# Performance work log

Measured on AMD Instinct MI355X. Metric: run time of the kernel, lower is better.

Reference implementation:

```python
import jax, jax.numpy as jnp
import numpy as np


def setup_inputs() -> dict:
    key = jax.random.key(0)
    k1, k2, k3 = jax.random.split(key, 3)
    B, C, S, D = 8, 256, 2048, 64
    a = jax.random.normal(k1, (B, C, S), dtype=jnp.float32)
    b = jax.random.normal(k2, (B, S, D), dtype=jnp.float32)
    c = jax.random.normal(k3, (B, S, D), dtype=jnp.float32)
    return {"a": a, "b": b, "c": c}


def reference(a, b, c):
    # mid[b, n, m] = softmax_m(b @ c^T), unscaled
    scores = jnp.einsum("bnd,bmd->bnm", b, c)
    mid = jax.nn.softmax(scores, axis=-1)  # [B, S, S]
    # out = a @ mid^T + a  -> [B, C, S]
    out = jnp.einsum("bcm,bnm->bcn", a, mid) + a
    return out
```

## Files before the change

### kernel.cpp

```cpp
#include <hip/hip_runtime.h>
#include <stdint.h>

#define S 2048
#define DHEAD 64
#define CDIM 256
#define NBATCH 8
#define NSTEP 32
#define SMT 8

typedef __attribute__((ext_vector_type(4))) float f32x4;
typedef __attribute__((ext_vector_type(8))) short s16x8;
typedef __attribute__((ext_vector_type(8))) _Float16 f16x8;
typedef __attribute__((ext_vector_type(4))) unsigned short u16x4;

static __device__ __forceinline__ unsigned short f2bf(float f) {
    unsigned int u = __builtin_bit_cast(unsigned int, f);
    unsigned int r = (u + 0x7FFFu + ((u >> 16) & 1u)) >> 16;
    return (unsigned short)r;
}
static __device__ __forceinline__ unsigned short f2h(float f) {
    _Float16 h = (_Float16)f;
    return __builtin_bit_cast(unsigned short, h);
}
static __device__ __forceinline__ float bf2f(unsigned short u) {
    return __builtin_bit_cast(float, (unsigned int)u << 16);
}

#define GLOAD16(g, l)                                                              \
    __builtin_amdgcn_global_load_lds(                                              \
        (const __attribute__((address_space(1))) void*)(g),                        \
        (__attribute__((address_space(3))) void*)(l), 16, 0, 0)

__global__ __launch_bounds__(256) void cvt_kernel(
    const float* __restrict__ a, const float* __restrict__ b, const float* __restrict__ c,
    unsigned short* __restrict__ a16, unsigned short* __restrict__ b16,
    unsigned short* __restrict__ c16)
{
    const int na4 = NBATCH * CDIM * S / 4;
    const int nbc4 = NBATCH * S * DHEAD / 4;
    int i0 = blockIdx.x * 256 + threadIdx.x;
    int stride = gridDim.x * 256;
    for (int i = i0; i < na4; i += stride) {
        f32x4 v = ((const f32x4*)a)[i];
        u16x4 o; o.x = f2bf(v.x); o.y = f2bf(v.y); o.z = f2bf(v.z); o.w = f2bf(v.w);
        ((u16x4*)a16)[i] = o;
    }
    for (int i = i0; i < nbc4; i += stride) {
        f32x4 v = ((const f32x4*)b)[i];
        u16x4 o; o.x = f2h(v.x); o.y = f2h(v.y); o.z = f2h(v.z); o.w = f2h(v.w);
        ((u16x4*)b16)[i] = o;
        f32x4 u = ((const f32x4*)c)[i];
        u16x4 p; p.x = f2h(u.x); p.y = f2h(u.y); p.z = f2h(u.z); p.w = f2h(u.w);
        ((u16x4*)c16)[i] = p;
    }
}

__global__ __launch_bounds__(256, 2) void scores_kernel(
    const unsigned short* __restrict__ B16, const unsigned short* __restrict__ C16,
    unsigned short* __restrict__ E, float* __restrict__ Lp, int b0, int nb)
{
    const int bid = blockIdx.x;
    int lb, idx;
    if (nb == 8) { lb = bid & 7; idx = bid >> 3; }
    else { lb = bid / 64; idx = bid - lb * 64; }
    const int gb = b0 + lb;
    const int nt = idx >> 1, mh = idx & 1;
    const int n0 = nt * 64;
    const int mbase = mh * (SMT * 128);

    const unsigned short* __restrict__ bp = B16 + (size_t)gb * S * DHEAD;
    const unsigned short* __restrict__ cp = C16 + (size_t)gb * S * DHEAD;
    unsigned short* __restrict__ Ep = E + (size_t)lb * S * S;

    __shared__ unsigned short bs[64 * 64];
    __shared__ unsigned short cs[2][128 * 64];
    __shared__ unsigned short es[64 * 136];
    __shared__ float Lsh[4 * 32];

    const int tid = threadIdx.x;
    const int lane = tid & 63;
    const int w = tid >> 6;
    const int wr = w >> 1, wc = w & 1;
    const int q = lane >> 4, r15 = lane & 15;

    int cRow[4], cOff[4], cR_[4], bRow[2], bOff[2], bR_[2];
    #pragma unroll
    for (int t = 0; t < 4; ++t) {
        int r = w + 4 * t, ch = r * 64 + lane;
        cR_[t] = r; cRow[t] = ch >> 3;
        cOff[t] = ((ch & 7) ^ ((ch >> 3) & 7)) * 8;
    }
    #pragma unroll
    for (int t = 0; t < 2; ++t) {
        int r = w + 4 * t, ch = r * 64 + lane;
        bR_[t] = r; bRow[t] = ch >> 3;
        bOff[t] = ((ch & 7) ^ ((ch >> 3) & 7)) * 8;
    }

#define SSTAGE_C(buf, m0)                                                          \
    {                                                                              \
        _Pragma("unroll")                                                          \
        for (int t = 0; t < 4; ++t)                                                \
            GLOAD16(cp + (size_t)((m0) + cRow[t]) * DHEAD + cOff[t],               \
                    &cs[buf][cR_[t] * 512]);                                       \
    }

    #pragma unroll
    for (int t = 0; t < 2; ++t)
        GLOAD16(bp + (size_t)(n0 + bRow[t]) * DHEAD + bOff[t], &bs[bR_[t] * 512]);
    SSTAGE_C(0, mbase);

    float sj[2] = {0.f, 0.f};

    #pragma unroll
    for (int mt = 0; mt < SMT; ++mt) {
        const int cur = mt & 1;
        const int m0 = mbase + mt * 128;
        if (mt < SMT - 1) {
            SSTAGE_C(cur ^ 1, m0 + 128);
            asm volatile("s_waitcnt vmcnt(4)" ::: "memory");
        } else {
            asm volatile("s_waitcnt vmcnt(0)" ::: "memory");
        }
        __builtin_amdgcn_sched_barrier(0);
        __builtin_amdgcn_s_barrier();
        __builtin_amdgcn_sched_barrier(0);

        f32x4 acc[4][2] = {};
        #pragma unroll
        for (int kk = 0; kk < 2; ++kk) {
            const int sz = ((kk * 4 + q) ^ (r15 & 7)) * 8;
            f16x8 af[4], bf[2];
            #pragma unroll
            for (int i = 0; i < 4; ++i)
                af[i] = *(const f16x8*)&cs[cur][(wr * 64 + i * 16 + r15) * 64 + sz];
            #pragma unroll
            for (int j = 0; j < 2; ++j)
                bf[j] = *(const f16x8*)&bs[(wc * 32 + j * 16 + r15) * 64 + sz];
            __builtin_amdgcn_s_setprio(1);
            #pragma unroll
            for (int i = 0; i < 4; ++i)
                #pragma unroll
                for (int j = 0; j < 2; ++j)
                    acc[i][j] = __builtin_amdgcn_mfma_f32_16x16x32_f16(af[i], bf[j], acc[i][j], 0, 0, 0);
            __builtin_amdgcn_s_setprio(0);
        }

        u16x4 pk[4][2];
        #pragma unroll
        for (int i = 0; i < 4; ++i)
            #pragma unroll
            for (int j = 0; j < 2; ++j) {
                float e0 = __expf(acc[i][j][0]);
                float e1 = __expf(acc[i][j][1]);
                float e2 = __expf(acc[i][j][2]);
                float e3 = __expf(acc[i][j][3]);
                sj[j] += (e0 + e1) + (e2 + e3);
                pk[i][j].x = f2bf(e0); pk[i][j].y = f2bf(e1);
                pk[i][j].z = f2bf(e2); pk[i][j].w = f2bf(e3);
            }

        __syncthreads();
        #pragma unroll
        for (int i = 0; i < 4; ++i)
            #pragma unroll
            for (int j = 0; j < 2; ++j) {
                int nl = wc * 32 + j * 16 + r15;
                int ml = wr * 64 + i * 16 + q * 4;
                *(u16x4*)&es[nl * 136 + ml] = pk[i][j];
            }
        __syncthreads();

        #pragma unroll
        for (int t = 0; t < 4; ++t) {
            int ch = tid + 256 * t;
            int row = ch >> 4, off = ch & 15;
            f32x4 v = *(const f32x4*)&es[row * 136 + off * 8];
            *(f32x4*)&Ep[(size_t)(n0 + row) * S + m0 + off * 8] = v;
        }
    }
#undef SSTAGE_C

    #pragma unroll
    for (int j = 0; j < 2; ++j) {
        sj[j] += __shfl_xor(sj[j], 16);
        sj[j] += __shfl_xor(sj[j], 32);
    }
    if (lane < 16) {
        Lsh[w * 32 + r15] = sj[0];
        Lsh[w * 32 + 16 + r15] = sj[1];
    }
    __syncthreads();
    if (tid < 64) {
        int wcn = tid >> 5, rem = tid & 31;
        float s = Lsh[wcn * 32 + rem] + Lsh[(2 + wcn) * 32 + rem];
        Lp[((size_t)lb * 2 + mh) * S + n0 + tid] = s;
    }
}

#define GEMM_DECODE()                                                             \
    const int tid = threadIdx.x;                                                  \
    const int lane = tid & 63;                                                    \
    const int w = tid >> 6;                                                       \
    const int wr = w >> 1, wc = w & 1;                                            \
    const int q = lane >> 4, r15 = lane & 15;                                     \
    int aRow[4], aOff[4], aR_[4], bRow[2], bOff[2], bR_[2];                       \
    _Pragma("unroll")                                                             \
    for (int t = 0; t < 4; ++t) {                                                 \
        int r = w + 4 * t, ch = r * 64 + lane;                                    \
        aR_[t] = r; aRow[t] = ch >> 3;                                            \
        aOff[t] = ((ch & 7) ^ ((ch >> 3) & 7)) * 8;                               \
    }                                                                             \
    _Pragma("unroll")                                                             \
    for (int t = 0; t < 2; ++t) {                                                 \
        int r = w + 4 * t, ch = r * 64 + lane;                                    \
        bR_[t] = r; bRow[t] = ch >> 3;                                            \
        bOff[t] = ((ch & 7) ^ ((ch >> 3) & 7)) * 8;                               \
    }

#define STAGEP(bufA, bufB, k0)                                                    \
    {                                                                             \
        _Pragma("unroll")                                                         \
        for (int t = 0; t < 4; ++t)                                               \
            GLOAD16(Ap + (size_t)(c0 + aRow[t]) * S + (k0) + aOff[t],             \
                    (bufA) + aR_[t] * 512);                                       \
        _Pragma("unroll")                                                         \
        for (int t = 0; t < 2; ++t)                                               \
            GLOAD16(Bp + (size_t)(n0 + bRow[t]) * S + (k0) + bOff[t],             \
                    (bufB) + bR_[t] * 512);                                       \
    }

#define GEMM_EPILOGUE()                                                           \
    float rcpL[2];                                                                \
    _Pragma("unroll")                                                             \
    for (int j = 0; j < 2; ++j) {                                                 \
        int n = n0 + wc * 32 + j * 16 + r15;                                      \
        float s = Lp[(size_t)lb * 2 * S + n] + Lp[((size_t)lb * 2 + 1) * S + n]; \
        rcpL[j] = 1.0f / s;                                                       \
    }                                                                             \
    _Pragma("unroll")                                                             \
    for (int i = 0; i < 4; ++i) {                                                 \
        _Pragma("unroll")                                                         \
        for (int rr = 0; rr < 4; ++rr) {                                          \
            int cc = c0 + wr * 64 + i * 16 + q * 4 + rr;                          \
            size_t base = (size_t)cc * S;                                         \
            _Pragma("unroll")                                                     \
            for (int j = 0; j < 2; ++j) {                                         \
                int n = n0 + wc * 32 + j * 16 + r15;                              \
                op[base + n] = acc[i][j][rr] * rcpL[j] + bf2f(Ap[base + n]);      \
            }                                                                     \
        }                                                                         \
    }

__global__ __launch_bounds__(256, 2) void gemm_kernel3(
    const unsigned short* __restrict__ a16, const unsigned short* __restrict__ E,
    const float* __restrict__ Lp, float* __restrict__ out, int b0, int nb)
{
    const int bid = blockIdx.x;
    int lb, idx;
    if (nb == 8) { lb = bid & 7; idx = bid >> 3; }
    else { lb = bid / 64; idx = bid - lb * 64; }
    const int gb = b0 + lb;
    const int nt = idx >> 1, ct = idx & 1;
    const int n0 = nt * 64, c0 = ct * 128;

    const unsigned short* __restrict__ Ap = a16 + (size_t)gb * CDIM * S;
    const unsigned short* __restrict__ Bp = E + (size_t)lb * S * S;
    float* __restrict__ op = out + (size_t)gb * CDIM * S;

    extern __shared__ char gsm[];
    unsigned short* As[3];
    unsigned short* Bs[3];
    #pragma unroll
    for (int u = 0; u < 3; ++u) {
        As[u] = (unsigned short*)gsm + u * (128 * 64 + 64 * 64);
        Bs[u] = As[u] + 128 * 64;
    }

    GEMM_DECODE();

    f32x4 acc[4][2] = {};

    STAGEP(As[0], Bs[0], 0);
    STAGEP(As[1], Bs[1], 64);

    const int sw0 = (q ^ (r15 & 7)) * 8;
    const int sw1 = ((4 + q) ^ (r15 & 7)) * 8;

    #pragma unroll
    for (int kt = 0; kt < NSTEP; ++kt) {
        const int cur = kt % 3;
        if (kt <= NSTEP - 3) {
            STAGEP(As[(kt + 2) % 3], Bs[(kt + 2) % 3], (kt + 2) * 64);
            asm volatile("s_waitcnt vmcnt(12)" ::: "memory");
        } else if (kt == NSTEP - 2) {
            asm volatile("s_waitcnt vmcnt(6)" ::: "memory");
        } else {
            asm volatile("s_waitcnt vmcnt(0)" ::: "memory");
        }
        __builtin_amdgcn_sched_barrier(0);
        __builtin_amdgcn_s_barrier();
        __builtin_amdgcn_sched_barrier(0);

        const unsigned short* Ar = As[cur];
        const unsigned short* Br = Bs[cur];
        #pragma unroll
        for (int kk = 0; kk < 2; ++kk) {
            const int sz = kk ? sw1 : sw0;
            s16x8 af[4], bf[2];
            #pragma unroll
            for (int i = 0; i < 4; ++i)
                af[i] = *(const s16x8*)&Ar[(wr * 64 + i * 16 + r15) * 64 + sz];
            #pragma unroll
            for (int j = 0; j < 2; ++j)
                bf[j] = *(const s16x8*)&Br[(wc * 32 + j * 16 + r15) * 64 + sz];
            __builtin_amdgcn_s_setprio(1);
            #pragma unroll
            for (int i = 0; i < 4; ++i)
                #pragma unroll
                for (int j = 0; j < 2; ++j)
                    acc[i][j] = __builtin_amdgcn_mfma_f32_16x16x32_bf16(af[i], bf[j], acc[i][j], 0, 0, 0);
            __builtin_amdgcn_s_setprio(0);
        }

        __builtin_amdgcn_sched_barrier(0);
        __builtin_amdgcn_s_barrier();
    }

    GEMM_EPILOGUE();
}

__global__ __launch_bounds__(256, 2) void gemm_kernel2(
    const unsigned short* __restrict__ a16, const unsigned short* __restrict__ E,
    const float* __restrict__ Lp, float* __restrict__ out, int b0, int nb)
{
    const int bid = blockIdx.x;
    int lb, idx;
    if (nb == 8) { lb = bid & 7; idx = bid >> 3; }
    else { lb = bid / 64; idx = bid - lb * 64; }
    const int gb = b0 + lb;
    const int nt = idx >> 1, ct = idx & 1;
    const int n0 = nt * 64, c0 = ct * 128;

    const unsigned short* __restrict__ Ap = a16 + (size_t)gb * CDIM * S;
    const unsigned short* __restrict__ Bp = E + (size_t)lb * S * S;
    float* __restrict__ op = out + (size_t)gb * CDIM * S;

    __shared__ unsigned short AsS[2][128 * 64];
    __shared__ unsigned short BsS[2][64 * 64];

    GEMM_DECODE();

    f32x4 acc[4][2] = {};

    STAGEP(AsS[0], BsS[0], 0);
    __syncthreads();

    const int sw0 = (q ^ (r15 & 7)) * 8;
    const int sw1 = ((4 + q) ^ (r15 & 7)) * 8;

    #pragma unroll 2
    for (int kt = 0; kt < NSTEP; ++kt) {
        const int cur = kt & 1;
        if (kt < NSTEP - 1) STAGEP(AsS[cur ^ 1], BsS[cur ^ 1], (kt + 1) * 64);

        #pragma unroll
        for (int kk = 0; kk < 2; ++kk) {
            const int sz = kk ? sw1 : sw0;
            s16x8 af[4], bf[2];
            #pragma unroll
            for (int i = 0; i < 4; ++i)
                af[i] = *(const s16x8*)&AsS[cur][(wr * 64 + i * 16 + r15) * 64 + sz];
            #pragma unroll
            for (int j = 0; j < 2; ++j)
                bf[j] = *(const s16x8*)&BsS[cur][(wc * 32 + j * 16 + r15) * 64 + sz];
            #pragma unroll
            for (int i = 0; i < 4; ++i)
                #pragma unroll
                for (int j = 0; j < 2; ++j)
                    acc[i][j] = __builtin_amdgcn_mfma_f32_16x16x32_bf16(af[i], bf[j], acc[i][j], 0, 0, 0);
        }
        __syncthreads();
    }

    GEMM_EPILOGUE();
}

extern "C" void kernel_launch(void* const* d_in, const int* in_sizes, int n_in,
                              void* d_out, int out_size, void* d_ws, size_t ws_size,
                              hipStream_t stream) {
    const float* a = (const float*)d_in[0];
    const float* b = (const float*)d_in[1];
    const float* c = (const float*)d_in[2];
    float* out = (float*)d_out;

    const size_t a16_bytes = (size_t)NBATCH * CDIM * S * 2;
    const size_t bc_bytes = (size_t)NBATCH * S * DHEAD * 2;
    const size_t head = a16_bytes + 2 * bc_bytes;
    const size_t perb = (size_t)S * S * 2 + (size_t)2 * S * 4;
    int G = 1;
    if (ws_size > head + perb) {
        size_t g = (ws_size - head) / perb;
        G = (g >= NBATCH) ? NBATCH : (int)g;
        if (G < 1) G = 1;
    }
    unsigned short* a16 = (unsigned short*)d_ws;
    unsigned short* b16 = (unsigned short*)((char*)d_ws + a16_bytes);
    unsigned short* c16 = (unsigned short*)((char*)d_ws + a16_bytes + bc_bytes);
    unsigned short* E = (unsigned short*)((char*)d_ws + head);
    float* Lp = (float*)((char*)d_ws + head + (size_t)G * S * S * 2);

    const int gemm_lds3 = 3 * (128 * 64 + 64 * 64) * 2;
    hipError_t attr_ok = hipFuncSetAttribute(
        reinterpret_cast<const void*>(gemm_kernel3),
        hipFuncAttributeMaxDynamicSharedMemorySize, gemm_lds3);

    cvt_kernel<<<1024, 256, 0, stream>>>(a, b, c, a16, b16, c16);

    for (int b0 = 0; b0 < NBATCH; b0 += G) {
        int nb = (NBATCH - b0 < G) ? (NBATCH - b0) : G;
        scores_kernel<<<64 * nb, 256, 0, stream>>>(b16, c16, E, Lp, b0, nb);
        if (attr_ok == hipSuccess)
            gemm_kernel3<<<64 * nb, 256, gemm_lds3, stream>>>(a16, E, Lp, out, b0, nb);
        else
            gemm_kernel2<<<64 * nb, 256, 0, stream>>>(a16, E, Lp, out, b0, nb);
    }
}
```

Before: 50.68 us.

## Replace GEMM with full-C wide-tile kernel using split-K waves and register A

Adds a 512-thread GEMM kernel in which each block covers all 256 C rows for a 64-column output tile, so each E tile is read once instead of twice. The A operand is loaded straight from global memory into registers and double-buffered there, while only the E tile is staged through a 3-deep LDS ring. The two wave groups each handle half of every K step, and their partial sums are reduced through LDS before the epilogue. This halves the grid and drops the old no-LDS fallback kernel, trading lower E traffic for larger register pressure, non-coalesced A loads and an added reduction step.

```diff
diff --git a/kernel.cpp b/kernel.cpp
--- a/kernel.cpp
+++ b/kernel.cpp
@@ -195,6 +195,123 @@
         int wcn = tid >> 5, rem = tid & 31;
         float s = Lsh[wcn * 32 + rem] + Lsh[(2 + wcn) * 32 + rem];
         Lp[((size_t)lb * 2 + mh) * S + n0 + tid] = s;
+    }
+}
+
+__global__ __launch_bounds__(512, 2) void gemm_kernelW(
+    const unsigned short* __restrict__ a16, const unsigned short* __restrict__ E,
+    const float* __restrict__ Lp, float* __restrict__ out, int b0, int nb)
+{
+    const int bid = blockIdx.x;
+    int lb, nt;
+    if (nb == 8) { lb = bid & 7; nt = bid >> 3; }
+    else { lb = bid / 32; nt = bid - lb * 32; }
+    const int gb = b0 + lb;
+    const int n0 = nt * 64;
+
+    const unsigned short* __restrict__ Ap = a16 + (size_t)gb * CDIM * S;
+    const unsigned short* __restrict__ Bp = E + (size_t)lb * S * S;
+    float* __restrict__ op = out + (size_t)gb * CDIM * S;
+
+    extern __shared__ char gsm[];
+    unsigned short* const Bbase = (unsigned short*)gsm;
+
+    const int tid = threadIdx.x;
+    const int lane = tid & 63;
+    const int w = tid >> 6;
+    const int wr = w & 3, ks = w >> 2;
+    const int q = lane >> 4, r15 = lane & 15;
+
+    const int brow = tid >> 3;
+    const int bsw = ((tid & 7) ^ (brow & 7)) * 8;
+    const size_t bgl = (size_t)(n0 + brow) * S + bsw;
+
+    size_t arow[4];
+    #pragma unroll
+    for (int i = 0; i < 4; ++i)
+        arow[i] = (size_t)(wr * 64 + i * 16 + r15) * S + ks * 32 + q * 8;
+
+    const int bsz = ((ks * 4 + q) ^ (r15 & 7)) * 8;
+
+    f32x4 acc[4][4] = {};
+    s16x8 af[2][4];
+
+    #pragma unroll
+    for (int i = 0; i < 4; ++i) af[0][i] = *(const s16x8*)&Ap[arow[i]];
+    GLOAD16(Bp + bgl, Bbase + w * 512);
+    #pragma unroll
+    for (int i = 0; i < 4; ++i) af[1][i] = *(const s16x8*)&Ap[arow[i] + 64];
+    GLOAD16(Bp + bgl + 64, Bbase + 4096 + w * 512);
+    __builtin_amdgcn_sched_barrier(0);
+
+    #pragma unroll
+    for (int kt = 0; kt < NSTEP; ++kt) {
+        if (kt < NSTEP - 1) asm volatile("s_waitcnt vmcnt(5)" ::: "memory");
+        else                asm volatile("s_waitcnt vmcnt(0)" ::: "memory");
+        __builtin_amdgcn_sched_barrier(0);
+        __builtin_amdgcn_s_barrier();
+        __builtin_amdgcn_sched_barrier(0);
+        if (kt + 2 < NSTEP)
+            GLOAD16(Bp + bgl + (kt + 2) * 64, Bbase + ((kt + 2) % 3) * 4096 + w * 512);
+        __builtin_amdgcn_sched_barrier(0);
+
+        const unsigned short* Br = Bbase + (kt % 3) * 4096;
+        s16x8 bf[4];
+        #pragma unroll
+        for (int j = 0; j < 4; ++j)
+            bf[j] = *(const s16x8*)&Br[(j * 16 + r15) * 64 + bsz];
+        __builtin_amdgcn_s_setprio(1);
+        #pragma unroll
+        for (int i = 0; i < 4; ++i)
+            #pragma unroll
+            for (int j = 0; j < 4; ++j)
+                acc[i][j] = __builtin_amdgcn_mfma_f32_16x16x32_bf16(af[kt & 1][i], bf[j], acc[i][j], 0, 0, 0);
+        __builtin_amdgcn_s_setprio(0);
+        __builtin_amdgcn_sched_barrier(0);
+        if (kt + 2 < NSTEP) {
+            #pragma unroll
+            for (int i = 0; i < 4; ++i)
+                af[kt & 1][i] = *(const s16x8*)&Ap[arow[i] + (kt + 2) * 64];
+        }
+        __builtin_amdgcn_sched_barrier(0);
+    }
+
+    __syncthreads();
+    f32x4* red = (f32x4*)gsm;
+    if (ks == 1) {
+        #pragma unroll
+        for (int i = 0; i < 4; ++i)
+            #pragma unroll
+            for (int j = 0; j < 4; ++j)
+                red[((i * 4 + j) * 4 + wr) * 64 + lane] = acc[i][j];
+    }
+    __syncthreads();
+    if (ks == 0) {
+        #pragma unroll
+        for (int i = 0; i < 4; ++i)
+            #pragma unroll
+            for (int j = 0; j < 4; ++j)
+                acc[i][j] += red[((i * 4 + j) * 4 + wr) * 64 + lane];
+
+        float rcpL[4];
+        #pragma unroll
+        for (int j = 0; j < 4; ++j) {
+            int n = n0 + j * 16 + r15;
+            float s = Lp[(size_t)lb * 2 * S + n] + Lp[((size_t)lb * 2 + 1) * S + n];
+            rcpL[j] = 1.0f / s;
+        }
+        #pragma unroll
+        for (int i = 0; i < 4; ++i)
+            #pragma unroll
+            for (int rr = 0; rr < 4; ++rr) {
+                int cc = wr * 64 + i * 16 + q * 4 + rr;
+                size_t base = (size_t)cc * S;
+                #pragma unroll
+                for (int j = 0; j < 4; ++j) {
+                    int n = n0 + j * 16 + r15;
+                    op[base + n] = acc[i][j][rr] * rcpL[j] + bf2f(Ap[base + n]);
+                }
+            }
     }
 }
 
@@ -230,28 +347,6 @@
                     (bufB) + bR_[t] * 512);                                       \
     }
 
-#define GEMM_EPILOGUE()                                                           \
-    float rcpL[2];                                                                \
-    _Pragma("unroll")                                                             \
-    for (int j = 0; j < 2; ++j) {                                                 \
-        int n = n0 + wc * 32 + j * 16 + r15;                                      \
-        float s = Lp[(size_t)lb * 2 * S + n] + Lp[((size_t)lb * 2 + 1) * S + n]; \
-        rcpL[j] = 1.0f / s;                                                       \
-    }                                                                             \
-    _Pragma("unroll")                                                             \
-    for (int i = 0; i < 4; ++i) {                                                 \
-        _Pragma("unroll")                                                         \
-        for (int rr = 0; rr < 4; ++rr) {                                          \
-            int cc = c0 + wr * 64 + i * 16 + q * 4 + rr;                          \
-            size_t base = (size_t)cc * S;                                         \
-            _Pragma("unroll")                                                     \
-            for (int j = 0; j < 2; ++j) {                                         \
-                int n = n0 + wc * 32 + j * 16 + r15;                              \
-                op[base + n] = acc[i][j][rr] * rcpL[j] + bf2f(Ap[base + n]);      \
-            }                                                                     \
-        }                                                                         \
-    }
-
 __global__ __launch_bounds__(256, 2) void gemm_kernel3(
     const unsigned short* __restrict__ a16, const unsigned short* __restrict__ E,
     const float* __restrict__ Lp, float* __restrict__ out, int b0, int nb)
@@ -327,63 +422,26 @@
         __builtin_amdgcn_s_barrier();
     }
 
-    GEMM_EPILOGUE();
-}
-
-__global__ __launch_bounds__(256, 2) void gemm_kernel2(
-    const unsigned short* __restrict__ a16, const unsigned short* __restrict__ E,
-    const float* __restrict__ Lp, float* __restrict__ out, int b0, int nb)
-{
-    const int bid = blockIdx.x;
-    int lb, idx;
-    if (nb == 8) { lb = bid & 7; idx = bid >> 3; }
-    else { lb = bid / 64; idx = bid - lb * 64; }
-    const int gb = b0 + lb;
-    const int nt = idx >> 1, ct = idx & 1;
-    const int n0 = nt * 64, c0 = ct * 128;
-
-    const unsigned short* __restrict__ Ap = a16 + (size_t)gb * CDIM * S;
-    const unsigned short* __restrict__ Bp = E + (size_t)lb * S * S;
-    float* __restrict__ op = out + (size_t)gb * CDIM * S;
-
-    __shared__ unsigned short AsS[2][128 * 64];
-    __shared__ unsigned short BsS[2][64 * 64];
-
-    GEMM_DECODE();
-
-    f32x4 acc[4][2] = {};
-
-    STAGEP(AsS[0], BsS[0], 0);
-    __syncthreads();
-
-    const int sw0 = (q ^ (r15 & 7)) * 8;
-    const int sw1 = ((4 + q) ^ (r15 & 7)) * 8;
-
-    #pragma unroll 2
-    for (int kt = 0; kt < NSTEP; ++kt) {
-        const int cur = kt & 1;
-        if (kt < NSTEP - 1) STAGEP(AsS[cur ^ 1], BsS[cur ^ 1], (kt + 1) * 64);
-
-        #pragma unroll
-        for (int kk = 0; kk < 2; ++kk) {
-            const int sz = kk ? sw1 : sw0;
-            s16x8 af[4], bf[2];
-            #pragma unroll
-            for (int i = 0; i < 4; ++i)
-                af[i] = *(const s16x8*)&AsS[cur][(wr * 64 + i * 16 + r15) * 64 + sz];
-            #pragma unroll
-            for (int j = 0; j < 2; ++j)
-                bf[j] = *(const s16x8*)&BsS[cur][(wc * 32 + j * 16 + r15) * 64 + sz];
-            #pragma unroll
-            for (int i = 0; i < 4; ++i)
-                #pragma unroll
-                for (int j = 0; j < 2; ++j)
-                    acc[i][j] = __builtin_amdgcn_mfma_f32_16x16x32_bf16(af[i], bf[j], acc[i][j], 0, 0, 0);
-        }
-        __syncthreads();
-    }
-
-    GEMM_EPILOGUE();
+    float rcpL[2];
+    #pragma unroll
+    for (int j = 0; j < 2; ++j) {
+        int n = n0 + wc * 32 + j * 16 + r15;
+        float s = Lp[(size_t)lb * 2 * S + n] + Lp[((size_t)lb * 2 + 1) * S + n];
+        rcpL[j] = 1.0f / s;
+    }
+    #pragma unroll
+    for (int i = 0; i < 4; ++i) {
+        #pragma unroll
+        for (int rr = 0; rr < 4; ++rr) {
+            int cc = c0 + wr * 64 + i * 16 + q * 4 + rr;
+            size_t base = (size_t)cc * S;
+            #pragma unroll
+            for (int j = 0; j < 2; ++j) {
+                int n = n0 + wc * 32 + j * 16 + r15;
+                op[base + n] = acc[i][j][rr] * rcpL[j] + bf2f(Ap[base + n]);
+            }
+        }
+    }
 }
 
 extern "C" void kernel_launch(void* const* d_in, const int* in_sizes, int n_in,
@@ -410,19 +468,25 @@
     unsigned short* E = (unsigned short*)((char*)d_ws + head);
     float* Lp = (float*)((char*)d_ws + head + (size_t)G * S * S * 2);
 
-    const int gemm_lds3 = 3 * (128 * 64 + 64 * 64) * 2;
-    hipError_t attr_ok = hipFuncSetAttribute(
-        reinterpret_cast<const void*>(gemm_kernel3),
-        hipFuncAttributeMaxDynamicSharedMemorySize, gemm_lds3);
+    const int ldsW = 65536;
+    hipError_t okW = hipFuncSetAttribute(
+        reinterpret_cast<const void*>(gemm_kernelW),
+        hipFuncAttributeMaxDynamicSharedMemorySize, ldsW);
+    const int lds3 = 3 * (128 * 64 + 64 * 64) * 2;
+    hipError_t ok3 = hipSuccess;
+    if (okW != hipSuccess)
+        ok3 = hipFuncSetAttribute(
+            reinterpret_cast<const void*>(gemm_kernel3),
+            hipFuncAttributeMaxDynamicSharedMemorySize, lds3);
 
     cvt_kernel<<<1024, 256, 0, stream>>>(a, b, c, a16, b16, c16);
 
     for (int b0 = 0; b0 < NBATCH; b0 += G) {
         int nb = (NBATCH - b0 < G) ? (NBATCH - b0) : G;
         scores_kernel<<<64 * nb, 256, 0, stream>>>(b16, c16, E, Lp, b0, nb);
-        if (attr_ok == hipSuccess)
-            gemm_kernel3<<<64 * nb, 256, gemm_lds3, stream>>>(a16, E, Lp, out, b0, nb);
-        else
-            gemm_kernel2<<<64 * nb, 256, 0, stream>>>(a16, E, Lp, out, b0, nb);
-    }
-}
+        if (okW == hipSuccess)
+            gemm_kernelW<<<32 * nb, 512, ldsW, stream>>>(a16, E, Lp, out, b0, nb);
+        else if (ok3 == hipSuccess)
+            gemm_kernel3<<<64 * nb, 256, lds3, stream>>>(a16, E, Lp, out, b0, nb);
+    }
+}
```

Result: slower. 70.43 us (+39.0%).
